# Performance work log

Hardware: AMD Instinct MI355X
Metric: run time of the kernel (lower is better)

Reference implementation:

```python
import jax, jax.numpy as jnp
import numpy as np

HIDDEN = 128
NUM_HEADS = 8
F32_MIN = jnp.finfo(jnp.float32).min


def _split_heads(x, n):
    # [B, S, D] -> [B, n, S, D//n]
    b, s, d = x.shape
    return x.reshape(b, s, n, d // n).transpose(0, 2, 1, 3)


def setup_inputs() -> dict:
    key = jax.random.key(0)
    k1, k2, k3 = jax.random.split(key, 3)
    B, S = 4, 2048
    key_and_value = jax.random.normal(k1, (B, S, 2 * HIDDEN), dtype=jnp.float32)
    query = jax.random.normal(k2, (B, S, HIDDEN), dtype=jnp.float32)
    seq_len = jax.random.randint(k3, (B, 1), 1, S + 1, dtype=jnp.int32)
    return {"key_and_value": key_and_value, "query": query, "seq_len": seq_len}


def reference(key_and_value, query, seq_len):
    B, S, _ = query.shape
    d_head = HIDDEN // NUM_HEADS
    k, v = jnp.split(key_and_value, 2, axis=2)           # each [B, S, HIDDEN]
    Q = _split_heads(query, NUM_HEADS) * (d_head ** 0.5)  # NOTE: original MULTIPLIES by sqrt(d_head)
    K = _split_heads(k, NUM_HEADS)
    V = _split_heads(v, NUM_HEADS)
    # scores: [B, H, S, S]
    logits = jnp.einsum('bhqd,bhkd->bhqk', Q, K)
    # length mask over key positions: valid where pos < seq_len (one-hot+cumsum trick)
    valid = (jnp.arange(S, dtype=jnp.int32)[None, :] < seq_len).astype(jnp.float32)  # [B, S]
    logits = logits + F32_MIN * (1.0 - valid[:, None, None, :])
    weights = jax.nn.softmax(logits, axis=-1)
    out = jnp.einsum('bhqk,bhkd->bhqd', weights, V)       # [B, H, S, d_head]
    return out.transpose(0, 2, 1, 3).reshape(B, S, HIDDEN)
```

## Files before the change

kernel.cpp:

```cpp
#include <hip/hip_runtime.h>
#include <hip/hip_bf16.h>

#define HIDDEN 128
#define NHEAD  8
#define DHEAD  16
#define KBLK   64
#define QBLK   64
#define CHUNK  512

typedef __attribute__((ext_vector_type(8))) __bf16 bf16x8;
typedef __attribute__((ext_vector_type(4))) __bf16 bf16x4;
typedef __attribute__((ext_vector_type(4))) float  f32x4;
typedef __attribute__((ext_vector_type(2))) float  f32x2;

#define LOG2E 1.44269504088896340736f

#define TR_READ(dst, addr, imm) \
    asm volatile("ds_read_b64_tr_b16 %0, %1 offset:" imm : "=v"(dst) : "v"(addr) : "memory")

__device__ __forceinline__ int permrow(int k) {
    return (k & 3) | (((k >> 3) & 3) << 2) | (((k >> 2) & 1) << 4) | ((k >> 5) << 5);
}

template<bool SPLIT>
__global__ __launch_bounds__(256, 8)
void mha_fwd(const float* __restrict__ kv,
             const float* __restrict__ q,
             const int*   __restrict__ seq_len,
             float* __restrict__ out,
             float* __restrict__ pbuf,
             float* __restrict__ mlbuf,
             int S, int nc)
{
    const int qtile = blockIdx.x;
    const int h     = blockIdx.y;
    int b, c0;
    if (SPLIT) { b = blockIdx.z / nc; c0 = blockIdx.z % nc; }
    else       { b = blockIdx.z;      c0 = 0; }
    const int L = seq_len[b];
    const int kstart = SPLIT ? c0 * CHUNK : 0;
    if (SPLIT && kstart >= L) return;
    const int kend = SPLIT ? min(L, kstart + CHUNK) : L;

    const int tid  = threadIdx.x;
    const int lane = tid & 63;
    const int wave = tid >> 6;
    const int g    = lane >> 4;
    const int lr   = lane & 15;

    __shared__ __bf16 Klds[KBLK][40];
    __shared__ __bf16 Vst[KBLK][16];
    __shared__ __bf16 Pst[4][16][72];

    const int qbase = qtile * QBLK + wave * 16;
    bf16x8 qfrag;
    {
        const float* qp = q + ((size_t)(b * S + qbase + lr) * HIDDEN) + h * DHEAD + (g & 1) * 8;
        #pragma unroll
        for (int j = 0; j < 8; ++j) {
            float qv = qp[j] * 4.0f;
            __bf16 hi = (__bf16)qv;
            qfrag[j] = (g < 2) ? hi : (__bf16)(qv - (float)hi);
        }
    }

    const int skey = tid >> 2;
    const int qd   = tid & 3;
    const int vrow = permrow(skey);
    const float* kbase = kv + ((size_t)(b * S + skey) * (2 * HIDDEN)) + h * DHEAD + 4 * qd;

    const unsigned vbase = (unsigned)(unsigned long long)(const void*)&Vst[0][0] + lane * 8;

    f32x4 acc = {0.f, 0.f, 0.f, 0.f};
    float m = -1e30f, lsum = 0.f;

    for (int kb = kstart; kb < kend; kb += KBLK) {
        __syncthreads();

        {
            const float* kp = kbase + (size_t)kb * (2 * HIDDEN);
            f32x4 kvec = *(const f32x4*)kp;
            f32x4 vvec = *(const f32x4*)(kp + HIDDEN);
            bf16x4 khv, klv, vv;
            #pragma unroll
            for (int i = 0; i < 4; ++i) {
                __bf16 hi = (__bf16)kvec[i];
                khv[i] = hi;
                klv[i] = (__bf16)(kvec[i] - (float)hi);
                vv[i]  = (__bf16)vvec[i];
            }
            *(bf16x4*)&Klds[skey][4 * qd]      = khv;
            *(bf16x4*)&Klds[skey][16 + 4 * qd] = klv;
            *(bf16x4*)&Vst[vrow][4 * qd]       = vv;
        }
        __syncthreads();

        f32x4 s[4];
        #pragma unroll
        for (int sub = 0; sub < 4; ++sub) {
            const __bf16* krow = &Klds[sub * 16 + lr][0];
            bf16x8 kf1 = *(const bf16x8*)&krow[(g & 1) * 8];
            bf16x8 kf2 = *(const bf16x8*)&krow[16 + (g & 1) * 8];
            f32x4 z = {0.f, 0.f, 0.f, 0.f};
            z = __builtin_amdgcn_mfma_f32_16x16x32_bf16(kf1, qfrag, z, 0, 0, 0);
            s[sub] = __builtin_amdgcn_mfma_f32_16x16x32_bf16(kf2, qfrag, z, 0, 0, 0);
        }

        if (kb + KBLK > kend) {
            #pragma unroll
            for (int sub = 0; sub < 4; ++sub)
                #pragma unroll
                for (int r = 0; r < 4; ++r)
                    if (kb + sub * 16 + g * 4 + r >= kend) s[sub][r] = -1e30f;
        }

        float t0 = fmaxf(fmaxf(s[0][0], s[0][1]), fmaxf(s[0][2], s[0][3]));
        float t1 = fmaxf(fmaxf(s[1][0], s[1][1]), fmaxf(s[1][2], s[1][3]));
        float t2 = fmaxf(fmaxf(s[2][0], s[2][1]), fmaxf(s[2][2], s[2][3]));
        float t3 = fmaxf(fmaxf(s[3][0], s[3][1]), fmaxf(s[3][2], s[3][3]));
        float tmax = fmaxf(fmaxf(t0, t1), fmaxf(t2, t3));
        tmax = fmaxf(tmax, __shfl_xor(tmax, 16));
        tmax = fmaxf(tmax, __shfl_xor(tmax, 32));

        const float mn = fmaxf(m, tmax);
        const float alpha = exp2f((m - mn) * LOG2E);
        m = mn;
        float rsum = 0.f;
        #pragma unroll
        for (int sub = 0; sub < 4; ++sub) {
            bf16x4 pk;
            #pragma unroll
            for (int r = 0; r < 4; ++r) {
                float p = exp2f((s[sub][r] - mn) * LOG2E);
                rsum += p;
                pk[r] = (__bf16)p;
            }
            *(bf16x4*)&Pst[wave][lr][sub * 16 + g * 4] = pk;
        }
        rsum += __shfl_xor(rsum, 16);
        rsum += __shfl_xor(rsum, 32);
        lsum = lsum * alpha + rsum;
        acc *= alpha;

        bf16x4 b0v, b1v, b2v, b3v;
        TR_READ(b0v, vbase, "0");
        TR_READ(b1v, vbase, "512");
        TR_READ(b2v, vbase, "1024");
        TR_READ(b3v, vbase, "1536");
        bf16x8 pa0 = *(const bf16x8*)&Pst[wave][lr][g * 8];
        bf16x8 pa1 = *(const bf16x8*)&Pst[wave][lr][32 + g * 8];
        asm volatile("s_waitcnt lgkmcnt(0)" ::: "memory");
        __builtin_amdgcn_sched_barrier(0);
        bf16x8 vb0, vb1;
        #pragma unroll
        for (int i = 0; i < 4; ++i) {
            vb0[i] = b0v[i]; vb0[i + 4] = b1v[i];
            vb1[i] = b2v[i]; vb1[i + 4] = b3v[i];
        }
        acc = __builtin_amdgcn_mfma_f32_16x16x32_bf16(vb0, pa0, acc, 0, 0, 0);
        acc = __builtin_amdgcn_mfma_f32_16x16x32_bf16(vb1, pa1, acc, 0, 0, 0);
    }

    const int qglob = qbase + lr;
    if (SPLIT) {
        const size_t row = (((size_t)b * nc + c0) * S + qglob) * NHEAD + h;
        *(f32x4*)&pbuf[row * DHEAD + g * 4] = acc;
        if (g == 0) { f32x2 ml = {m, lsum}; *(f32x2*)&mlbuf[row * 2] = ml; }
    } else {
        const float inv = 1.0f / lsum;
        *(f32x4*)&out[((size_t)b * S + qglob) * HIDDEN + h * DHEAD + g * 4] = acc * inv;
    }
}

__global__ __launch_bounds__(256)
void mha_merge(const float* __restrict__ pbuf, const float* __restrict__ mlbuf,
               const int* __restrict__ seq_len, float* __restrict__ out, int S, int nc)
{
    const int t = blockIdx.x * 256 + threadIdx.x;
    const int h = t & (NHEAD - 1);
    const int rest = t >> 3;
    const int qg = rest % S;
    const int b  = rest / S;
    const int L  = seq_len[b];
    const int nch = (L + CHUNK - 1) / CHUNK;

    const size_t cstr = (size_t)S * NHEAD;
    const size_t row0 = ((size_t)b * nc) * cstr + (size_t)qg * NHEAD + h;

    float mv[8], lv[8];
    float M = -1e30f;
    for (int c = 0; c < nch; ++c) {
        f32x2 ml = *(const f32x2*)&mlbuf[(row0 + c * cstr) * 2];
        mv[c] = ml[0]; lv[c] = ml[1];
        M = fmaxf(M, ml[0]);
    }
    float den = 0.f;
    f32x4 o0 = {0,0,0,0}, o1 = o0, o2 = o0, o3 = o0;
    for (int c = 0; c < nch; ++c) {
        float w = exp2f((mv[c] - M) * LOG2E);
        den += w * lv[c];
        const float* pp = &pbuf[(row0 + c * cstr) * DHEAD];
        o0 += w * *(const f32x4*)&pp[0];
        o1 += w * *(const f32x4*)&pp[4];
        o2 += w * *(const f32x4*)&pp[8];
        o3 += w * *(const f32x4*)&pp[12];
    }
    const float inv = 1.0f / den;
    float* op = &out[((size_t)b * S + qg) * HIDDEN + h * DHEAD];
    *(f32x4*)&op[0]  = o0 * inv;
    *(f32x4*)&op[4]  = o1 * inv;
    *(f32x4*)&op[8]  = o2 * inv;
    *(f32x4*)&op[12] = o3 * inv;
}

extern "C" void kernel_launch(void* const* d_in, const int* in_sizes, int n_in,
                              void* d_out, int out_size, void* d_ws, size_t ws_size,
                              hipStream_t stream)
{
    const float* kv      = (const float*)d_in[0];
    const float* query   = (const float*)d_in[1];
    const int*   seq_len = (const int*)d_in[2];
    float* out           = (float*)d_out;

    const int B = in_sizes[2];
    const int S = in_sizes[1] / (B * HIDDEN);
    const int nc = (S + CHUNK - 1) / CHUNK;

    const size_t pbytes  = (size_t)B * nc * S * NHEAD * DHEAD * sizeof(float);
    const size_t mlbytes = (size_t)B * nc * S * NHEAD * 2 * sizeof(float);

    if (ws_size >= pbytes + mlbytes && nc <= 8) {
        float* pbuf  = (float*)d_ws;
        float* mlbuf = (float*)((char*)d_ws + pbytes);
        dim3 grid(S / QBLK, NHEAD, B * nc);
        mha_fwd<true><<<grid, dim3(256), 0, stream>>>(kv, query, seq_len, nullptr, pbuf, mlbuf, S, nc);
        const int nrows = B * S * NHEAD;
        mha_merge<<<dim3((nrows + 255) / 256), dim3(256), 0, stream>>>(pbuf, mlbuf, seq_len, out, S, nc);
    } else {
        dim3 grid(S / QBLK, NHEAD, B);
        mha_fwd<false><<<grid, dim3(256), 0, stream>>>(kv, query, seq_len, out, nullptr, nullptr, S, 1);
    }
}
```

Before: 46.43 us.

## Add K/V bf16 prepass kernel and double-buffered async LDS staging in attention

Adds a prepass kernel that converts K into hi/lo bf16 splits and V into a transposed, swizzled bf16 tile layout once per (batch, head, key block), written to workspace. The main attention kernel then streams these pre-formatted tiles into double-buffered LDS with global_load_lds while computing the current block. This removes repeated per-query-tile fp32-to-bf16 conversion and the transpose reads, and overlaps loads with compute. LOG2E is folded into the query scale. The cost is an extra kernel launch and workspace traffic, plus more LDS per block, which may lower occupancy.

```diff
diff --git a/kernel.cpp b/kernel.cpp
--- a/kernel.cpp
+++ b/kernel.cpp
@@ -7,26 +7,134 @@
 #define KBLK   64
 #define QBLK   64
 #define CHUNK  512
+#define TILEB  6144
+#define QSCALE 5.77078016355585277626f
 
 typedef __attribute__((ext_vector_type(8))) __bf16 bf16x8;
 typedef __attribute__((ext_vector_type(4))) __bf16 bf16x4;
 typedef __attribute__((ext_vector_type(4))) float  f32x4;
 typedef __attribute__((ext_vector_type(2))) float  f32x2;
 
-#define LOG2E 1.44269504088896340736f
-
 #define TR_READ(dst, addr, imm) \
     asm volatile("ds_read_b64_tr_b16 %0, %1 offset:" imm : "=v"(dst) : "v"(addr) : "memory")
 
+#define GL16(gsrc, ldsoff) \
+    __builtin_amdgcn_global_load_lds((const __attribute__((address_space(1))) unsigned int*)(gsrc), \
+        (__attribute__((address_space(3))) unsigned int*)(unsigned)(ldsoff), 16, 0, 0)
+
 __device__ __forceinline__ int permrow(int k) {
     return (k & 3) | (((k >> 3) & 3) << 2) | (((k >> 2) & 1) << 4) | ((k >> 5) << 5);
 }
 
-template<bool SPLIT>
+__global__ __launch_bounds__(256, 4)
+void mha_prepass(const float* __restrict__ kv, char* __restrict__ kbuf, int S)
+{
+    const int t    = blockIdx.x;
+    const int b    = blockIdx.y;
+    const int zh   = blockIdx.z;
+    const int lane = threadIdx.x & 63;
+    const int wave = threadIdx.x >> 6;
+    const int h    = zh * 4 + wave;
+    const int k    = lane;
+
+    __shared__ __align__(16) __bf16 Vw[4][64][16];
+
+    const float* kp = kv + ((size_t)(b * S + t * KBLK + k) * (2 * HIDDEN)) + h * DHEAD;
+    char* tb = kbuf + (((size_t)(b * NHEAD + h) * (S / KBLK)) + t) * TILEB;
+
+    f32x4 k0 = *(const f32x4*)(kp + 0);
+    f32x4 k1 = *(const f32x4*)(kp + 4);
+    f32x4 k2 = *(const f32x4*)(kp + 8);
+    f32x4 k3 = *(const f32x4*)(kp + 12);
+    bf16x8 hiA, hiB, loA, loB;
+    #pragma unroll
+    for (int i = 0; i < 4; ++i) {
+        __bf16 h0 = (__bf16)k0[i]; hiA[i]     = h0; loA[i]     = (__bf16)(k0[i] - (float)h0);
+        __bf16 h1 = (__bf16)k1[i]; hiA[i + 4] = h1; loA[i + 4] = (__bf16)(k1[i] - (float)h1);
+        __bf16 h2 = (__bf16)k2[i]; hiB[i]     = h2; loB[i]     = (__bf16)(k2[i] - (float)h2);
+        __bf16 h3 = (__bf16)k3[i]; hiB[i + 4] = h3; loB[i + 4] = (__bf16)(k3[i] - (float)h3);
+    }
+    const int ka = (k >> 4) * 512 + (k & 15) * 16;
+    *(bf16x8*)(tb + ka)              = hiA;
+    *(bf16x8*)(tb + ka + 256)        = hiB;
+    *(bf16x8*)(tb + 2048 + ka)       = loA;
+    *(bf16x8*)(tb + 2048 + ka + 256) = loB;
+
+    const float* vp = kp + HIDDEN;
+    f32x4 v0 = *(const f32x4*)(vp + 0);
+    f32x4 v1 = *(const f32x4*)(vp + 4);
+    f32x4 v2 = *(const f32x4*)(vp + 8);
+    f32x4 v3 = *(const f32x4*)(vp + 12);
+    bf16x8 va, vb;
+    #pragma unroll
+    for (int i = 0; i < 4; ++i) {
+        va[i] = (__bf16)v0[i]; va[i + 4] = (__bf16)v1[i];
+        vb[i] = (__bf16)v2[i]; vb[i + 4] = (__bf16)v3[i];
+    }
+    const int pr = permrow(k);
+    *(bf16x8*)&Vw[wave][pr][0] = va;
+    *(bf16x8*)&Vw[wave][pr][8] = vb;
+
+    const unsigned vbase = (unsigned)(unsigned long long)(const void*)&Vw[wave][0][0] + lane * 8;
+    bf16x4 t0v, t1v, t2v, t3v;
+    TR_READ(t0v, vbase, "0");
+    TR_READ(t1v, vbase, "512");
+    TR_READ(t2v, vbase, "1024");
+    TR_READ(t3v, vbase, "1536");
+    asm volatile("s_waitcnt lgkmcnt(0)" ::: "memory");
+    __builtin_amdgcn_sched_barrier(0);
+    bf16x8 w0, w1;
+    #pragma unroll
+    for (int i = 0; i < 4; ++i) {
+        w0[i] = t0v[i]; w0[i + 4] = t1v[i];
+        w1[i] = t2v[i]; w1[i + 4] = t3v[i];
+    }
+    const int lr = lane & 15, g = lane >> 4, sw = (lr & 7) << 4;
+    char* vt = tb + 4096 + lr * 128;
+    *(bf16x8*)(vt + ((g * 16) ^ sw))      = w0;
+    *(bf16x8*)(vt + ((64 + g * 16) ^ sw)) = w1;
+}
+
+__device__ __forceinline__ void stage_pre(const char* tile, unsigned ldsoff, int wave, int lane)
+{
+    const char* gp = tile + lane * 16;
+    if (wave == 0)      { GL16(gp,        ldsoff);        GL16(gp + 1024, ldsoff + 1024); }
+    else if (wave == 1) { GL16(gp + 2048, ldsoff + 2048); GL16(gp + 3072, ldsoff + 3072); }
+    else if (wave == 2) { GL16(gp + 4096, ldsoff + 4096); }
+    else                { GL16(gp + 5120, ldsoff + 5120); }
+}
+
+__device__ __forceinline__ void stage_raw(const float* kv, int b, int S, int h, int kb,
+                                          char* Sb, int tid)
+{
+    const int skey = tid >> 2, qd = tid & 3;
+    const float* kp = kv + ((size_t)(b * S + kb + skey) * (2 * HIDDEN)) + h * DHEAD + 4 * qd;
+    f32x4 kvec = *(const f32x4*)kp;
+    f32x4 vvec = *(const f32x4*)(kp + HIDDEN);
+    bf16x4 khv, klv;
+    #pragma unroll
+    for (int i = 0; i < 4; ++i) {
+        __bf16 hi = (__bf16)kvec[i];
+        khv[i] = hi;
+        klv[i] = (__bf16)(kvec[i] - (float)hi);
+    }
+    const int ahi = (skey >> 4) * 512 + (qd >> 1) * 256 + (skey & 15) * 16 + (qd & 1) * 8;
+    *(bf16x4*)(Sb + ahi)        = khv;
+    *(bf16x4*)(Sb + 2048 + ahi) = klv;
+    #pragma unroll
+    for (int i = 0; i < 4; ++i) {
+        const int d = 4 * qd + i;
+        const int addr = 4096 + d * 128 + (((skey >> 3) * 16) ^ ((d & 7) << 4)) + (skey & 7) * 2;
+        *(__bf16*)(Sb + addr) = (__bf16)vvec[i];
+    }
+}
+
+template<bool SPLIT, bool PRE>
 __global__ __launch_bounds__(256, 8)
 void mha_fwd(const float* __restrict__ kv,
              const float* __restrict__ q,
              const int*   __restrict__ seq_len,
+             const char*  __restrict__ kbuf,
              float* __restrict__ out,
              float* __restrict__ pbuf,
              float* __restrict__ mlbuf,
@@ -47,10 +155,10 @@
     const int wave = tid >> 6;
     const int g    = lane >> 4;
     const int lr   = lane & 15;
-
-    __shared__ __bf16 Klds[KBLK][40];
-    __shared__ __bf16 Vst[KBLK][16];
-    __shared__ __bf16 Pst[4][16][72];
+    const int sw   = (lr & 7) << 4;
+
+    __shared__ __align__(16) char   Stg[2][TILEB];
+    __shared__ __align__(16) __bf16 Pst[4][16][72];
 
     const int qbase = qtile * QBLK + wave * 16;
     bf16x8 qfrag;
@@ -58,49 +166,47 @@
         const float* qp = q + ((size_t)(b * S + qbase + lr) * HIDDEN) + h * DHEAD + (g & 1) * 8;
         #pragma unroll
         for (int j = 0; j < 8; ++j) {
-            float qv = qp[j] * 4.0f;
+            float qv = qp[j] * QSCALE;
             __bf16 hi = (__bf16)qv;
             qfrag[j] = (g < 2) ? hi : (__bf16)(qv - (float)hi);
         }
     }
 
-    const int skey = tid >> 2;
-    const int qd   = tid & 3;
-    const int vrow = permrow(skey);
-    const float* kbase = kv + ((size_t)(b * S + skey) * (2 * HIDDEN)) + h * DHEAD + 4 * qd;
-
-    const unsigned vbase = (unsigned)(unsigned long long)(const void*)&Vst[0][0] + lane * 8;
+    const unsigned stg0 = (unsigned)(unsigned long long)(const void*)&Stg[0][0];
+    const char* tcur = PRE ? kbuf + (((size_t)(b * NHEAD + h) * (S / KBLK)) + (kstart >> 6)) * TILEB
+                           : nullptr;
 
     f32x4 acc = {0.f, 0.f, 0.f, 0.f};
     float m = -1e30f, lsum = 0.f;
+    int cur = 0;
+
+    if constexpr (PRE) stage_pre(tcur, stg0, wave, lane);
+    else               stage_raw(kv, b, S, h, kstart, &Stg[0][0], tid);
 
     for (int kb = kstart; kb < kend; kb += KBLK) {
-        __syncthreads();
-
-        {
-            const float* kp = kbase + (size_t)kb * (2 * HIDDEN);
-            f32x4 kvec = *(const f32x4*)kp;
-            f32x4 vvec = *(const f32x4*)(kp + HIDDEN);
-            bf16x4 khv, klv, vv;
-            #pragma unroll
-            for (int i = 0; i < 4; ++i) {
-                __bf16 hi = (__bf16)kvec[i];
-                khv[i] = hi;
-                klv[i] = (__bf16)(kvec[i] - (float)hi);
-                vv[i]  = (__bf16)vvec[i];
+        const bool hasnext = (kb + KBLK) < kend;
+        if constexpr (PRE) {
+            if (hasnext) {
+                stage_pre(tcur + TILEB, stg0 + (unsigned)((cur ^ 1) * TILEB), wave, lane);
+                if (wave < 2) asm volatile("s_waitcnt vmcnt(2)" ::: "memory");
+                else          asm volatile("s_waitcnt vmcnt(1)" ::: "memory");
+            } else {
+                asm volatile("s_waitcnt vmcnt(0)" ::: "memory");
             }
-            *(bf16x4*)&Klds[skey][4 * qd]      = khv;
-            *(bf16x4*)&Klds[skey][16 + 4 * qd] = klv;
-            *(bf16x4*)&Vst[vrow][4 * qd]       = vv;
-        }
-        __syncthreads();
+            __builtin_amdgcn_s_barrier();
+            __builtin_amdgcn_sched_barrier(0);
+        } else {
+            if (hasnext) stage_raw(kv, b, S, h, kb + KBLK, &Stg[cur ^ 1][0], tid);
+            __syncthreads();
+        }
+
+        const char* Sb = &Stg[cur][0];
 
         f32x4 s[4];
         #pragma unroll
         for (int sub = 0; sub < 4; ++sub) {
-            const __bf16* krow = &Klds[sub * 16 + lr][0];
-            bf16x8 kf1 = *(const bf16x8*)&krow[(g & 1) * 8];
-            bf16x8 kf2 = *(const bf16x8*)&krow[16 + (g & 1) * 8];
+            bf16x8 kf1 = *(const bf16x8*)(Sb + sub * 512 + (g & 1) * 256 + lr * 16);
+            bf16x8 kf2 = *(const bf16x8*)(Sb + 2048 + sub * 512 + (g & 1) * 256 + lr * 16);
             f32x4 z = {0.f, 0.f, 0.f, 0.f};
             z = __builtin_amdgcn_mfma_f32_16x16x32_bf16(kf1, qfrag, z, 0, 0, 0);
             s[sub] = __builtin_amdgcn_mfma_f32_16x16x32_bf16(kf2, qfrag, z, 0, 0, 0);
@@ -123,7 +229,7 @@
         tmax = fmaxf(tmax, __shfl_xor(tmax, 32));
 
         const float mn = fmaxf(m, tmax);
-        const float alpha = exp2f((m - mn) * LOG2E);
+        const float alpha = exp2f(m - mn);
         m = mn;
         float rsum = 0.f;
         #pragma unroll
@@ -131,7 +237,7 @@
             bf16x4 pk;
             #pragma unroll
             for (int r = 0; r < 4; ++r) {
-                float p = exp2f((s[sub][r] - mn) * LOG2E);
+                float p = exp2f(s[sub][r] - mn);
                 rsum += p;
                 pk[r] = (__bf16)p;
             }
@@ -142,23 +248,21 @@
         lsum = lsum * alpha + rsum;
         acc *= alpha;
 
-        bf16x4 b0v, b1v, b2v, b3v;
-        TR_READ(b0v, vbase, "0");
-        TR_READ(b1v, vbase, "512");
-        TR_READ(b2v, vbase, "1024");
-        TR_READ(b3v, vbase, "1536");
+        bf16x8 vb0 = *(const bf16x8*)(Sb + 4096 + lr * 128 + ((g * 16) ^ sw));
+        bf16x8 vb1 = *(const bf16x8*)(Sb + 4096 + lr * 128 + ((64 + g * 16) ^ sw));
         bf16x8 pa0 = *(const bf16x8*)&Pst[wave][lr][g * 8];
         bf16x8 pa1 = *(const bf16x8*)&Pst[wave][lr][32 + g * 8];
-        asm volatile("s_waitcnt lgkmcnt(0)" ::: "memory");
-        __builtin_amdgcn_sched_barrier(0);
-        bf16x8 vb0, vb1;
-        #pragma unroll
-        for (int i = 0; i < 4; ++i) {
-            vb0[i] = b0v[i]; vb0[i + 4] = b1v[i];
-            vb1[i] = b2v[i]; vb1[i + 4] = b3v[i];
-        }
         acc = __builtin_amdgcn_mfma_f32_16x16x32_bf16(vb0, pa0, acc, 0, 0, 0);
         acc = __builtin_amdgcn_mfma_f32_16x16x32_bf16(vb1, pa1, acc, 0, 0, 0);
+
+        if constexpr (PRE) {
+            __builtin_amdgcn_s_barrier();
+            __builtin_amdgcn_sched_barrier(0);
+        } else {
+            __syncthreads();
+        }
+        cur ^= 1;
+        if constexpr (PRE) tcur += TILEB;
     }
 
     const int qglob = qbase + lr;
@@ -197,7 +301,7 @@
     float den = 0.f;
     f32x4 o0 = {0,0,0,0}, o1 = o0, o2 = o0, o3 = o0;
     for (int c = 0; c < nch; ++c) {
-        float w = exp2f((mv[c] - M) * LOG2E);
+        float w = exp2f(mv[c] - M);
         den += w * lv[c];
         const float* pp = &pbuf[(row0 + c * cstr) * DHEAD];
         o0 += w * *(const f32x4*)&pp[0];
@@ -226,18 +330,33 @@
     const int S = in_sizes[1] / (B * HIDDEN);
     const int nc = (S + CHUNK - 1) / CHUNK;
 
-    const size_t pbytes  = (size_t)B * nc * S * NHEAD * DHEAD * sizeof(float);
-    const size_t mlbytes = (size_t)B * nc * S * NHEAD * 2 * sizeof(float);
-
-    if (ws_size >= pbytes + mlbytes && nc <= 8) {
-        float* pbuf  = (float*)d_ws;
-        float* mlbuf = (float*)((char*)d_ws + pbytes);
-        dim3 grid(S / QBLK, NHEAD, B * nc);
-        mha_fwd<true><<<grid, dim3(256), 0, stream>>>(kv, query, seq_len, nullptr, pbuf, mlbuf, S, nc);
+    const size_t preb = (size_t)B * NHEAD * (S / KBLK) * TILEB;
+    const size_t pb   = (size_t)B * nc * S * NHEAD * DHEAD * sizeof(float);
+    const size_t mlb  = (size_t)B * nc * S * NHEAD * 2 * sizeof(float);
+
+    if (nc <= 8 && ws_size >= preb + pb + mlb) {
+        char*  kbuf  = (char*)d_ws;
+        float* pbuf  = (float*)((char*)d_ws + preb);
+        float* mlbuf = (float*)((char*)d_ws + preb + pb);
+        mha_prepass<<<dim3(S / KBLK, B, 2), dim3(256), 0, stream>>>(kv, (char*)kbuf, S);
+        mha_fwd<true, true><<<dim3(S / QBLK, NHEAD, B * nc), dim3(256), 0, stream>>>(
+            kv, query, seq_len, kbuf, nullptr, pbuf, mlbuf, S, nc);
         const int nrows = B * S * NHEAD;
         mha_merge<<<dim3((nrows + 255) / 256), dim3(256), 0, stream>>>(pbuf, mlbuf, seq_len, out, S, nc);
+    } else if (nc <= 8 && ws_size >= pb + mlb) {
+        float* pbuf  = (float*)d_ws;
+        float* mlbuf = (float*)((char*)d_ws + pb);
+        mha_fwd<true, false><<<dim3(S / QBLK, NHEAD, B * nc), dim3(256), 0, stream>>>(
+            kv, query, seq_len, nullptr, nullptr, pbuf, mlbuf, S, nc);
+        const int nrows = B * S * NHEAD;
+        mha_merge<<<dim3((nrows + 255) / 256), dim3(256), 0, stream>>>(pbuf, mlbuf, seq_len, out, S, nc);
+    } else if (ws_size >= preb) {
+        char* kbuf = (char*)d_ws;
+        mha_prepass<<<dim3(S / KBLK, B, 2), dim3(256), 0, stream>>>(kv, kbuf, S);
+        mha_fwd<false, true><<<dim3(S / QBLK, NHEAD, B), dim3(256), 0, stream>>>(
+            kv, query, seq_len, kbuf, out, nullptr, nullptr, S, 1);
     } else {
-        dim3 grid(S / QBLK, NHEAD, B);
-        mha_fwd<false><<<grid, dim3(256), 0, stream>>>(kv, query, seq_len, out, nullptr, nullptr, S, 1);
-    }
-}
+        mha_fwd<false, false><<<dim3(S / QBLK, NHEAD, B), dim3(256), 0, stream>>>(
+            kv, query, seq_len, nullptr, out, nullptr, nullptr, S, 1);
+    }
+}
```

Result: slower. 52.89 us (+13.9%).

## Double-buffer K/V staging and keep P in registers with swizzled LDS layout

Applied to the files above, without the earlier changes.

Replaces the two-barrier-per-tile K/V staging with a double-buffered LDS ring: the next tile's global loads are issued before the current tile's compute, and are converted and stored after it, leaving one barrier per tile. The K and V layouts are reorganised (swizzled V rows, permuted key order) so the P fragments come straight from the score registers, which drops the P round-trip through LDS and the transpose reads. It also folds log2(e) into the Q scale so the exponentials skip a multiply. The cost is twice the LDS and a lower occupancy hint (launch bounds 8 to 4 waves), and the permuted key order must stay consistent with the masking.

```diff
diff --git a/kernel.cpp b/kernel.cpp
--- a/kernel.cpp
+++ b/kernel.cpp
@@ -7,23 +7,38 @@
 #define KBLK   64
 #define QBLK   64
 #define CHUNK  512
+#define TILEB  6144
+#define QSCALE 5.77078016355585277626f
 
 typedef __attribute__((ext_vector_type(8))) __bf16 bf16x8;
 typedef __attribute__((ext_vector_type(4))) __bf16 bf16x4;
 typedef __attribute__((ext_vector_type(4))) float  f32x4;
 typedef __attribute__((ext_vector_type(2))) float  f32x2;
-
-#define LOG2E 1.44269504088896340736f
-
-#define TR_READ(dst, addr, imm) \
-    asm volatile("ds_read_b64_tr_b16 %0, %1 offset:" imm : "=v"(dst) : "v"(addr) : "memory")
-
-__device__ __forceinline__ int permrow(int k) {
-    return (k & 3) | (((k >> 3) & 3) << 2) | (((k >> 2) & 1) << 4) | ((k >> 5) << 5);
+typedef __attribute__((ext_vector_type(4))) int    i32x4;
+
+__device__ __forceinline__ int ksub(int k)  { return ((k >> 5) << 1) | ((k >> 2) & 1); }
+__device__ __forceinline__ int kirow(int k) { return (((k >> 3) & 3) << 2) | (k & 3); }
+
+
+__device__ __forceinline__ void cvt_store(char* Sb, int ka, i32x4 vaddr,
+                                          f32x4 kvec, f32x4 vvec)
+{
+    bf16x4 khv, klv;
+    #pragma unroll
+    for (int i = 0; i < 4; ++i) {
+        __bf16 hi = (__bf16)kvec[i];
+        khv[i] = hi;
+        klv[i] = (__bf16)(kvec[i] - (float)hi);
+    }
+    *(bf16x4*)(Sb + ka)        = khv;
+    *(bf16x4*)(Sb + 2048 + ka) = klv;
+    #pragma unroll
+    for (int i = 0; i < 4; ++i)
+        *(__bf16*)(Sb + vaddr[i]) = (__bf16)vvec[i];
 }
 
 template<bool SPLIT>
-__global__ __launch_bounds__(256, 8)
+__global__ __launch_bounds__(256, 4)
 void mha_fwd(const float* __restrict__ kv,
              const float* __restrict__ q,
              const int*   __restrict__ seq_len,
@@ -47,10 +62,9 @@
     const int wave = tid >> 6;
     const int g    = lane >> 4;
     const int lr   = lane & 15;
-
-    __shared__ __bf16 Klds[KBLK][40];
-    __shared__ __bf16 Vst[KBLK][16];
-    __shared__ __bf16 Pst[4][16][72];
+    const int sw   = (lr & 7) << 4;
+
+    __shared__ __align__(16) char Stg[2][TILEB];
 
     const int qbase = qtile * QBLK + wave * 16;
     bf16x8 qfrag;
@@ -58,60 +72,72 @@
         const float* qp = q + ((size_t)(b * S + qbase + lr) * HIDDEN) + h * DHEAD + (g & 1) * 8;
         #pragma unroll
         for (int j = 0; j < 8; ++j) {
-            float qv = qp[j] * 4.0f;
+            float qv = qp[j] * QSCALE;
             __bf16 hi = (__bf16)qv;
             qfrag[j] = (g < 2) ? hi : (__bf16)(qv - (float)hi);
         }
     }
 
-    const int skey = tid >> 2;
-    const int qd   = tid & 3;
-    const int vrow = permrow(skey);
-    const float* kbase = kv + ((size_t)(b * S + skey) * (2 * HIDDEN)) + h * DHEAD + 4 * qd;
-
-    const unsigned vbase = (unsigned)(unsigned long long)(const void*)&Vst[0][0] + lane * 8;
+    const int sk = tid >> 2;
+    const int qd = tid & 3;
+    const float* kvp = kv + ((size_t)(b * S + sk) * (2 * HIDDEN)) + h * DHEAD + 4 * qd;
+    const int ka = ksub(sk) * 512 + (qd >> 1) * 256 + kirow(sk) * 16 + (qd & 1) * 8;
+    i32x4 vaddr;
+    #pragma unroll
+    for (int i = 0; i < 4; ++i) {
+        const int d = 4 * qd + i;
+        vaddr[i] = 4096 + d * 128 + (((sk >> 3) * 16) ^ ((d & 7) << 4)) + (sk & 7) * 2;
+    }
 
     f32x4 acc = {0.f, 0.f, 0.f, 0.f};
     float m = -1e30f, lsum = 0.f;
 
-    for (int kb = kstart; kb < kend; kb += KBLK) {
-        __syncthreads();
-
-        {
-            const float* kp = kbase + (size_t)kb * (2 * HIDDEN);
-            f32x4 kvec = *(const f32x4*)kp;
-            f32x4 vvec = *(const f32x4*)(kp + HIDDEN);
-            bf16x4 khv, klv, vv;
-            #pragma unroll
-            for (int i = 0; i < 4; ++i) {
-                __bf16 hi = (__bf16)kvec[i];
-                khv[i] = hi;
-                klv[i] = (__bf16)(kvec[i] - (float)hi);
-                vv[i]  = (__bf16)vvec[i];
-            }
-            *(bf16x4*)&Klds[skey][4 * qd]      = khv;
-            *(bf16x4*)&Klds[skey][16 + 4 * qd] = klv;
-            *(bf16x4*)&Vst[vrow][4 * qd]       = vv;
-        }
-        __syncthreads();
+    const int ntiles = (kend - kstart + KBLK - 1) >> 6;
+
+    {
+        const float* kp = kvp + (size_t)kstart * (2 * HIDDEN);
+        f32x4 kvec = *(const f32x4*)kp;
+        f32x4 vvec = *(const f32x4*)(kp + HIDDEN);
+        cvt_store(&Stg[0][0], ka, vaddr, kvec, vvec);
+    }
+    __syncthreads();
+
+    for (int ti = 0; ti < ntiles; ++ti) {
+        const int kb = kstart + ti * KBLK;
+        const char* Sb = &Stg[ti & 1][0];
+        const bool hasnext = (ti + 1) < ntiles;
+
+        f32x4 nkv, nvv;
+        if (hasnext) {
+            const float* kp = kvp + (size_t)(kb + KBLK) * (2 * HIDDEN);
+            nkv = *(const f32x4*)kp;
+            nvv = *(const f32x4*)(kp + HIDDEN);
+        }
+
+        bf16x8 kfh[4], kfl[4];
+        #pragma unroll
+        for (int sub = 0; sub < 4; ++sub) {
+            kfh[sub] = *(const bf16x8*)(Sb + sub * 512 + (g & 1) * 256 + lr * 16);
+            kfl[sub] = *(const bf16x8*)(Sb + 2048 + sub * 512 + (g & 1) * 256 + lr * 16);
+        }
+        bf16x8 vb0 = *(const bf16x8*)(Sb + 4096 + lr * 128 + ((g * 16) ^ sw));
+        bf16x8 vb1 = *(const bf16x8*)(Sb + 4096 + lr * 128 + ((64 + g * 16) ^ sw));
 
         f32x4 s[4];
         #pragma unroll
         for (int sub = 0; sub < 4; ++sub) {
-            const __bf16* krow = &Klds[sub * 16 + lr][0];
-            bf16x8 kf1 = *(const bf16x8*)&krow[(g & 1) * 8];
-            bf16x8 kf2 = *(const bf16x8*)&krow[16 + (g & 1) * 8];
             f32x4 z = {0.f, 0.f, 0.f, 0.f};
-            z = __builtin_amdgcn_mfma_f32_16x16x32_bf16(kf1, qfrag, z, 0, 0, 0);
-            s[sub] = __builtin_amdgcn_mfma_f32_16x16x32_bf16(kf2, qfrag, z, 0, 0, 0);
-        }
-
+            z = __builtin_amdgcn_mfma_f32_16x16x32_bf16(kfh[sub], qfrag, z, 0, 0, 0);
+            s[sub] = __builtin_amdgcn_mfma_f32_16x16x32_bf16(kfl[sub], qfrag, z, 0, 0, 0);
+        }
         if (kb + KBLK > kend) {
             #pragma unroll
-            for (int sub = 0; sub < 4; ++sub)
+            for (int sub = 0; sub < 4; ++sub) {
+                const int kb2 = kb + (sub >> 1) * 32 + (sub & 1) * 4 + g * 8;
                 #pragma unroll
                 for (int r = 0; r < 4; ++r)
-                    if (kb + sub * 16 + g * 4 + r >= kend) s[sub][r] = -1e30f;
+                    if (kb2 + r >= kend) s[sub][r] = -1e30f;
+            }
         }
 
         float t0 = fmaxf(fmaxf(s[0][0], s[0][1]), fmaxf(s[0][2], s[0][3]));
@@ -123,42 +149,38 @@
         tmax = fmaxf(tmax, __shfl_xor(tmax, 32));
 
         const float mn = fmaxf(m, tmax);
-        const float alpha = exp2f((m - mn) * LOG2E);
+        const float alpha = exp2f(m - mn);
         m = mn;
+
         float rsum = 0.f;
-        #pragma unroll
-        for (int sub = 0; sub < 4; ++sub) {
-            bf16x4 pk;
+        bf16x8 pa0, pa1;
+        #pragma unroll
+        for (int sub = 0; sub < 2; ++sub)
             #pragma unroll
             for (int r = 0; r < 4; ++r) {
-                float p = exp2f((s[sub][r] - mn) * LOG2E);
+                float p = exp2f(s[sub][r] - mn);
                 rsum += p;
-                pk[r] = (__bf16)p;
+                pa0[sub * 4 + r] = (__bf16)p;
             }
-            *(bf16x4*)&Pst[wave][lr][sub * 16 + g * 4] = pk;
-        }
+        #pragma unroll
+        for (int sub = 2; sub < 4; ++sub)
+            #pragma unroll
+            for (int r = 0; r < 4; ++r) {
+                float p = exp2f(s[sub][r] - mn);
+                rsum += p;
+                pa1[(sub - 2) * 4 + r] = (__bf16)p;
+            }
         rsum += __shfl_xor(rsum, 16);
         rsum += __shfl_xor(rsum, 32);
         lsum = lsum * alpha + rsum;
         acc *= alpha;
 
-        bf16x4 b0v, b1v, b2v, b3v;
-        TR_READ(b0v, vbase, "0");
-        TR_READ(b1v, vbase, "512");
-        TR_READ(b2v, vbase, "1024");
-        TR_READ(b3v, vbase, "1536");
-        bf16x8 pa0 = *(const bf16x8*)&Pst[wave][lr][g * 8];
-        bf16x8 pa1 = *(const bf16x8*)&Pst[wave][lr][32 + g * 8];
-        asm volatile("s_waitcnt lgkmcnt(0)" ::: "memory");
-        __builtin_amdgcn_sched_barrier(0);
-        bf16x8 vb0, vb1;
-        #pragma unroll
-        for (int i = 0; i < 4; ++i) {
-            vb0[i] = b0v[i]; vb0[i + 4] = b1v[i];
-            vb1[i] = b2v[i]; vb1[i + 4] = b3v[i];
-        }
         acc = __builtin_amdgcn_mfma_f32_16x16x32_bf16(vb0, pa0, acc, 0, 0, 0);
         acc = __builtin_amdgcn_mfma_f32_16x16x32_bf16(vb1, pa1, acc, 0, 0, 0);
+
+        if (hasnext)
+            cvt_store(&Stg[(ti + 1) & 1][0], ka, vaddr, nkv, nvv);
+        __syncthreads();
     }
 
     const int qglob = qbase + lr;
@@ -197,7 +219,7 @@
     float den = 0.f;
     f32x4 o0 = {0,0,0,0}, o1 = o0, o2 = o0, o3 = o0;
     for (int c = 0; c < nch; ++c) {
-        float w = exp2f((mv[c] - M) * LOG2E);
+        float w = exp2f(mv[c] - M);
         den += w * lv[c];
         const float* pp = &pbuf[(row0 + c * cstr) * DHEAD];
         o0 += w * *(const f32x4*)&pp[0];
@@ -226,18 +248,18 @@
     const int S = in_sizes[1] / (B * HIDDEN);
     const int nc = (S + CHUNK - 1) / CHUNK;
 
-    const size_t pbytes  = (size_t)B * nc * S * NHEAD * DHEAD * sizeof(float);
-    const size_t mlbytes = (size_t)B * nc * S * NHEAD * 2 * sizeof(float);
-
-    if (ws_size >= pbytes + mlbytes && nc <= 8) {
+    const size_t pb  = (size_t)B * nc * S * NHEAD * DHEAD * sizeof(float);
+    const size_t mlb = (size_t)B * nc * S * NHEAD * 2 * sizeof(float);
+
+    if (nc <= 8 && ws_size >= pb + mlb) {
         float* pbuf  = (float*)d_ws;
-        float* mlbuf = (float*)((char*)d_ws + pbytes);
-        dim3 grid(S / QBLK, NHEAD, B * nc);
-        mha_fwd<true><<<grid, dim3(256), 0, stream>>>(kv, query, seq_len, nullptr, pbuf, mlbuf, S, nc);
+        float* mlbuf = (float*)((char*)d_ws + pb);
+        mha_fwd<true><<<dim3(S / QBLK, NHEAD, B * nc), dim3(256), 0, stream>>>(
+            kv, query, seq_len, nullptr, pbuf, mlbuf, S, nc);
         const int nrows = B * S * NHEAD;
         mha_merge<<<dim3((nrows + 255) / 256), dim3(256), 0, stream>>>(pbuf, mlbuf, seq_len, out, S, nc);
     } else {
-        dim3 grid(S / QBLK, NHEAD, B);
-        mha_fwd<false><<<grid, dim3(256), 0, stream>>>(kv, query, seq_len, out, nullptr, nullptr, S, 1);
-    }
-}
+        mha_fwd<false><<<dim3(S / QBLK, NHEAD, B), dim3(256), 0, stream>>>(
+            kv, query, seq_len, out, nullptr, nullptr, S, 1);
+    }
+}
```

Result: faster. 45.00 us (-3.1%).
